# Kernel optimization log

Measured on AMD Instinct MI355X. Metric: run time of the kernel, lower is better.

## Reference

```python
import jax, jax.numpy as jnp
import numpy as np

N_NODES = 100000


def gcn_conv(x, src, dst, norm, W, b, n_nodes):
    # PyG GCNConv: h = x @ W; out[i] = sum_{j->i} norm_ij * h[j]; out += b
    h = x @ W  # [N, F_out]
    msg = h[src] * norm[:, None]  # [E+N, F_out] gather + scale
    out = jax.ops.segment_sum(msg, dst, num_segments=n_nodes)
    return out + b


def setup_inputs() -> dict:
    key = jax.random.key(0)
    ks = jax.random.split(key, 5)
    n, e = N_NODES, 1600000
    d_in, d_h, d_out = 512, 128, 40
    x = jax.random.normal(ks[0], (n, d_in), dtype=jnp.float32)
    edge_index = jax.random.randint(ks[1], (2, e), 0, n, dtype=jnp.int64)
    # Glorot-ish scaled weights
    W1 = jax.random.normal(ks[2], (d_in, d_h), dtype=jnp.float32) * (1.0 / np.sqrt(d_in))
    b1 = jnp.zeros((d_h,), dtype=jnp.float32)
    W2 = jax.random.normal(ks[3], (d_h, d_out), dtype=jnp.float32) * (1.0 / np.sqrt(d_h))
    b2 = jnp.zeros((d_out,), dtype=jnp.float32)
    return {"x": x, "edge_index": edge_index, "W1": W1, "b1": b1, "W2": W2, "b2": b2}


def reference(x, edge_index, W1, b1, W2, b2):
    n = x.shape[0]
    # add self-loops (PyG default add_self_loops=True)
    loop = jnp.arange(n, dtype=edge_index.dtype)
    src = jnp.concatenate([edge_index[0], loop])
    dst = jnp.concatenate([edge_index[1], loop])
    # symmetric normalization: deg^-1/2[src] * deg^-1/2[dst]
    deg = jax.ops.segment_sum(jnp.ones_like(dst, dtype=x.dtype), dst, num_segments=n)
    dinv = jnp.where(deg > 0, jax.lax.rsqrt(jnp.maximum(deg, 1.0)), 0.0)
    norm = dinv[src] * dinv[dst]
    h = gcn_conv(x, src, dst, norm, W1, b1, n)
    h = jax.nn.relu(h)
    h = gcn_conv(h, src, dst, norm, W2, b2, n)
    return jax.nn.log_softmax(h, axis=1)
```

## Files before the change

kernel.cpp:

```cpp
#include <hip/hip_runtime.h>
#include <math.h>

#define SCAN_B 512
#define NBSHIFT 8
#define CHUNK 8192

typedef __attribute__((ext_vector_type(8))) short short8;
typedef __attribute__((ext_vector_type(4))) float v4f;

__device__ __forceinline__ unsigned short f2bf(float f) {
    unsigned int u = __float_as_uint(f);
    u += 0x7FFFu + ((u >> 16) & 1u);
    return (unsigned short)(u >> 16);
}
__device__ __forceinline__ unsigned int packbf(float a, float b) {
    return (unsigned int)f2bf(a) | ((unsigned int)f2bf(b) << 16);
}
__device__ __forceinline__ void bf8_to_f32(uint4 v, float* f) {
    f[0] = __uint_as_float(v.x << 16); f[1] = __uint_as_float(v.x & 0xFFFF0000u);
    f[2] = __uint_as_float(v.y << 16); f[3] = __uint_as_float(v.y & 0xFFFF0000u);
    f[4] = __uint_as_float(v.z << 16); f[5] = __uint_as_float(v.z & 0xFFFF0000u);
    f[6] = __uint_as_float(v.w << 16); f[7] = __uint_as_float(v.w & 0xFFFF0000u);
}

__global__ void count_deg_kernel(const int* __restrict__ dst, int E, int* __restrict__ counts) {
    int e = blockIdx.x * blockDim.x + threadIdx.x;
    if (e < E) atomicAdd(&counts[dst[e]], 1);
}

__global__ void scan1_kernel(const int* __restrict__ counts, int N,
                             int* __restrict__ partial, int* __restrict__ blockSums) {
    __shared__ int sm[SCAN_B];
    int tid = threadIdx.x;
    int i = blockIdx.x * SCAN_B + tid;
    int v = (i < N) ? counts[i] : 0;
    sm[tid] = v;
    __syncthreads();
    for (int off = 1; off < SCAN_B; off <<= 1) {
        int t = (tid >= off) ? sm[tid - off] : 0;
        __syncthreads();
        sm[tid] += t;
        __syncthreads();
    }
    if (i < N) partial[i] = sm[tid] - v;
    if (tid == SCAN_B - 1) blockSums[blockIdx.x] = sm[tid];
}

__global__ void scan2_kernel(int* __restrict__ blockSums, int nb) {
    __shared__ int sm[256];
    int tid = threadIdx.x;
    int v = (tid < nb) ? blockSums[tid] : 0;
    sm[tid] = v;
    __syncthreads();
    for (int off = 1; off < 256; off <<= 1) {
        int t = (tid >= off) ? sm[tid - off] : 0;
        __syncthreads();
        sm[tid] += t;
        __syncthreads();
    }
    if (tid < nb) blockSums[tid] = sm[tid] - v;
}

__global__ void scan3_kernel(const int* __restrict__ counts, int* __restrict__ offsets,
                             const int* __restrict__ blockSums, int N, int E,
                             int* __restrict__ cursor, float* __restrict__ dinv) {
    int i = blockIdx.x * SCAN_B + threadIdx.x;
    if (i < N) {
        int off = offsets[i] + blockSums[blockIdx.x];
        offsets[i] = off;
        cursor[i] = off;
        dinv[i] = rsqrtf((float)(counts[i] + 1));
    }
    if (i == 0 && blockIdx.x == 0) offsets[N] = E;
}

__global__ void binbase_kernel(const int* __restrict__ offsets, int* __restrict__ bin_base,
                               int* __restrict__ bin_cursor, int nbins, int N) {
    int b = blockIdx.x * 256 + threadIdx.x;
    if (b <= nbins) {
        int node = b << NBSHIFT;
        if (node > N) node = N;
        bin_base[b] = offsets[node];
        if (b < nbins) bin_cursor[b] = offsets[node];
    }
}

__global__ __launch_bounds__(256) void binpass_kernel(const int* __restrict__ src,
                                                      const int* __restrict__ dst, int E,
                                                      int* __restrict__ bin_cursor,
                                                      unsigned int* __restrict__ bpairs, int nbins) {
    __shared__ unsigned int pk[CHUNK];
    __shared__ unsigned short binOf[CHUNK];
    __shared__ int hist[512];
    __shared__ int scanned[512];
    __shared__ int rank[512];
    __shared__ int gbase[512];
    int tid = threadIdx.x;
    int base = blockIdx.x * CHUNK;
    int cnt = E - base; if (cnt > CHUNK) cnt = CHUNK;

    for (int i = tid; i < 512; i += 256) { hist[i] = 0; rank[i] = 0; }
    __syncthreads();
    for (int i = tid; i < cnt; i += 256) {
        int d = dst[base + i];
        atomicAdd(&hist[d >> NBSHIFT], 1);
    }
    __syncthreads();
    scanned[tid] = hist[tid]; scanned[tid + 256] = hist[tid + 256];
    __syncthreads();
    for (int off = 1; off < 512; off <<= 1) {
        int i0 = tid, i1 = tid + 256;
        int v0 = (i0 >= off) ? scanned[i0 - off] : 0;
        int v1 = (i1 >= off) ? scanned[i1 - off] : 0;
        __syncthreads();
        scanned[i0] += v0; scanned[i1] += v1;
        __syncthreads();
    }
    for (int i = tid; i < cnt; i += 256) {
        int d = dst[base + i];
        int s = src[base + i];
        int b = d >> NBSHIFT;
        unsigned int p = (unsigned int)s | ((unsigned int)(d & 255) << 17);
        int r = atomicAdd(&rank[b], 1);
        int pos = scanned[b] - hist[b] + r;
        pk[pos] = p;
        binOf[pos] = (unsigned short)b;
    }
    __syncthreads();
    for (int b = tid; b < nbins; b += 256)
        if (hist[b] > 0) gbase[b] = atomicAdd(&bin_cursor[b], hist[b]);
    __syncthreads();
    for (int i = tid; i < cnt; i += 256) {
        int b = binOf[i];
        int local = i - (scanned[b] - hist[b]);
        bpairs[gbase[b] + local] = pk[i];
    }
}

__global__ __launch_bounds__(256) void binscatter_kernel(const unsigned int* __restrict__ bpairs,
                                                         const int* __restrict__ bin_base,
                                                         int* __restrict__ cursor,
                                                         int* __restrict__ ssrc) {
    int b = blockIdx.x;
    int start = bin_base[b], end = bin_base[b + 1];
    int dhigh = b << NBSHIFT;
    for (int i = start + threadIdx.x; i < end; i += 256) {
        unsigned int p = bpairs[i];
        int s = (int)(p & 0x1FFFFu);
        int d = dhigh | (int)(p >> 17);
        int pos = atomicAdd(&cursor[d], 1);
        ssrc[pos] = s;
    }
}

__global__ void w1cast_kernel(const float* __restrict__ W1, unsigned short* __restrict__ W1s) {
    int idx = blockIdx.x * 256 + threadIdx.x;
    int k = idx >> 7, n = idx & 127;
    int dstIdx = ((k >> 6) << 13) | (n << 6) | ((((k >> 3) & 7) ^ (n & 7)) << 3) | (k & 7);
    W1s[dstIdx] = f2bf(W1[idx]);
}

#define BM1 128
#define BK1 64

__global__ __launch_bounds__(256) void gemm1_mfma_kernel(const float* __restrict__ X,
                                                         const unsigned short* __restrict__ W1s,
                                                         unsigned short* __restrict__ H, int N) {
    __shared__ unsigned short SMEM[16384];
    unsigned short* As = SMEM;
    unsigned short* Bs = SMEM + 8192;
    int tid = threadIdx.x;
    int wave = tid >> 6, lane = tid & 63;
    int quad = lane >> 4, lr = lane & 15;
    int mBase = (wave & 1) * 64, nBase = (wave >> 1) * 64;
    int rowBase = blockIdx.x * BM1;

    v4f zero4 = {0.f, 0.f, 0.f, 0.f};
    v4f acc[4][4];
    #pragma unroll
    for (int i = 0; i < 4; i++)
        #pragma unroll
        for (int j = 0; j < 4; j++) acc[i][j] = zero4;

    float4 pfA0[4], pfA1[4];
    uint4  pfB[4];

    #define LOAD_A(K0)                                                                  \
        _Pragma("unroll")                                                               \
        for (int t = 0; t < 4; t++) {                                                   \
            int idx = tid + t * 256;                                                    \
            int r = idx >> 3, c = idx & 7;                                              \
            int gr = rowBase + r;                                                       \
            const float4* p = (const float4*)(X + (size_t)gr * 512 + (K0) + c * 8);     \
            bool ok = gr < N;                                                           \
            pfA0[t] = ok ? p[0] : make_float4(0.f, 0.f, 0.f, 0.f);                      \
            pfA1[t] = ok ? p[1] : make_float4(0.f, 0.f, 0.f, 0.f);                      \
        }
    #define LOAD_B(K0)                                                                  \
        _Pragma("unroll")                                                               \
        for (int t = 0; t < 4; t++)                                                     \
            pfB[t] = *(const uint4*)(W1s + (((K0) >> 6) << 13) + ((tid + t * 256) << 3));

    LOAD_A(0); LOAD_B(0);

    for (int k0 = 0; k0 < 512; k0 += BK1) {
        __syncthreads();
        #pragma unroll
        for (int t = 0; t < 4; t++) {
            int idx = tid + t * 256;
            int r = idx >> 3, c = idx & 7;
            uint4 v;
            v.x = packbf(pfA0[t].x, pfA0[t].y); v.y = packbf(pfA0[t].z, pfA0[t].w);
            v.z = packbf(pfA1[t].x, pfA1[t].y); v.w = packbf(pfA1[t].z, pfA1[t].w);
            *(uint4*)(&As[(r << 6) + ((c ^ (r & 7)) << 3)]) = v;
        }
        #pragma unroll
        for (int t = 0; t < 4; t++)
            *(uint4*)(&Bs[(tid + t * 256) << 3]) = pfB[t];
        __syncthreads();
        if (k0 + BK1 < 512) { LOAD_A(k0 + BK1); LOAD_B(k0 + BK1); }
        #pragma unroll
        for (int kc = 0; kc < BK1; kc += 32) {
            int cb = kc >> 3;
            short8 aF[4], bF[4];
            #pragma unroll
            for (int i = 0; i < 4; i++) {
                int m = mBase + i * 16 + lr;
                aF[i] = *(const short8*)(&As[m * 64 + (((cb + quad) ^ (m & 7)) << 3)]);
            }
            #pragma unroll
            for (int j = 0; j < 4; j++) {
                int n = nBase + j * 16 + lr;
                bF[j] = *(const short8*)(&Bs[n * 64 + (((cb + quad) ^ (n & 7)) << 3)]);
            }
            #pragma unroll
            for (int i = 0; i < 4; i++)
                #pragma unroll
                for (int j = 0; j < 4; j++)
                    acc[i][j] = __builtin_amdgcn_mfma_f32_16x16x32_bf16(aF[i], bF[j], acc[i][j], 0, 0, 0);
        }
    }
    __syncthreads();
    unsigned short* Cs = SMEM;
    #pragma unroll
    for (int i = 0; i < 4; i++) {
        #pragma unroll
        for (int r = 0; r < 4; r++) {
            int m = mBase + i * 16 + quad * 4 + r;
            #pragma unroll
            for (int j = 0; j < 4; j++)
                Cs[m * 128 + ((nBase + j * 16 + lr) ^ ((m & 7) << 4))] = f2bf(acc[i][j][r]);
        }
    }
    __syncthreads();
    #pragma unroll
    for (int t = 0; t < 8; t++) {
        int idx = tid + t * 256;
        int row = idx >> 4, c = idx & 15;
        int gr = rowBase + row;
        if (gr < N)
            *(uint4*)(H + (size_t)gr * 128 + c * 8) =
                *(const uint4*)(&Cs[row * 128 + ((c * 8) ^ ((row & 7) << 4))]);
    }
    #undef LOAD_A
    #undef LOAD_B
}

__global__ __launch_bounds__(256) void agg1_kernel(const unsigned short* __restrict__ h1,
                                                   const int* __restrict__ offsets,
                                                   const int* __restrict__ ssrc,
                                                   const float* __restrict__ dinv,
                                                   const float* __restrict__ bias,
                                                   unsigned short* __restrict__ a1, int N) {
    int lane = threadIdx.x & 15;
    int node = (blockIdx.x << 4) + (threadIdx.x >> 4);
    if (node >= N) return;
    const uint4* h = (const uint4*)h1;
    float di = dinv[node];
    float acc[8], t[8];
    bf8_to_f32(h[(size_t)node * 16 + lane], t);
    #pragma unroll
    for (int i = 0; i < 8; i++) acc[i] = di * t[i];
    int e = offsets[node], e1 = offsets[node + 1];
    for (; e + 3 < e1; e += 4) {
        int sA = ssrc[e], sB = ssrc[e + 1], sC = ssrc[e + 2], sD = ssrc[e + 3];
        float wA = dinv[sA], wB = dinv[sB], wC = dinv[sC], wD = dinv[sD];
        uint4 vA = h[(size_t)sA * 16 + lane];
        uint4 vB = h[(size_t)sB * 16 + lane];
        uint4 vC = h[(size_t)sC * 16 + lane];
        uint4 vD = h[(size_t)sD * 16 + lane];
        float fA[8], fB[8], fC[8], fD[8];
        bf8_to_f32(vA, fA); bf8_to_f32(vB, fB); bf8_to_f32(vC, fC); bf8_to_f32(vD, fD);
        #pragma unroll
        for (int i = 0; i < 8; i++) {
            acc[i] = fmaf(wA, fA[i], acc[i]);
            acc[i] = fmaf(wB, fB[i], acc[i]);
            acc[i] = fmaf(wC, fC[i], acc[i]);
            acc[i] = fmaf(wD, fD[i], acc[i]);
        }
    }
    for (; e < e1; e++) {
        int s = ssrc[e];
        float w = dinv[s];
        float fs[8];
        bf8_to_f32(h[(size_t)s * 16 + lane], fs);
        #pragma unroll
        for (int i = 0; i < 8; i++) acc[i] = fmaf(w, fs[i], acc[i]);
    }
    float4 b0 = ((const float4*)bias)[lane * 2];
    float4 b1v = ((const float4*)bias)[lane * 2 + 1];
    float bb[8] = {b0.x, b0.y, b0.z, b0.w, b1v.x, b1v.y, b1v.z, b1v.w};
    float o[8];
    #pragma unroll
    for (int i = 0; i < 8; i++) o[i] = fmaxf(fmaf(di, acc[i], bb[i]), 0.f);
    uint4 pv;
    pv.x = packbf(o[0], o[1]); pv.y = packbf(o[2], o[3]);
    pv.z = packbf(o[4], o[5]); pv.w = packbf(o[6], o[7]);
    ((uint4*)a1)[(size_t)node * 16 + lane] = pv;
}

__global__ __launch_bounds__(256) void gemm2_kernel(const unsigned short* __restrict__ A,
                                                    const float* __restrict__ W,
                                                    float* __restrict__ H, int N) {
    __shared__ float As2[128][64];
    __shared__ float Ws[128 * 40];
    int tid = threadIdx.x;
    int rowBase = blockIdx.x * 64;

    #pragma unroll
    for (int l = 0; l < 4; l++) {
        int e = tid + l * 256;
        int r = e >> 4;
        int kk = (e & 15) << 3;
        int grow = rowBase + r;
        float f[8] = {0.f, 0.f, 0.f, 0.f, 0.f, 0.f, 0.f, 0.f};
        if (grow < N) {
            uint4 v = *(const uint4*)(A + (size_t)grow * 128 + kk);
            bf8_to_f32(v, f);
        }
        #pragma unroll
        for (int q = 0; q < 8; q++) As2[kk + q][r] = f[q];
    }
    #pragma unroll
    for (int l = 0; l < 5; l++) {
        int e = tid + l * 256;
        *(float4*)&Ws[e << 2] = *(const float4*)&W[e << 2];
    }
    __syncthreads();

    int tx = tid & 7;
    int ty = tid >> 3;
    float acc[2][5];
    #pragma unroll
    for (int r = 0; r < 2; r++)
        #pragma unroll
        for (int c = 0; c < 5; c++) acc[r][c] = 0.f;

    #pragma unroll 8
    for (int k = 0; k < 128; k++) {
        float a0 = As2[k][ty * 2];
        float a1v = As2[k][ty * 2 + 1];
        #pragma unroll
        for (int c = 0; c < 5; c++) {
            float w = Ws[k * 40 + tx * 5 + c];
            acc[0][c] = fmaf(a0, w, acc[0][c]);
            acc[1][c] = fmaf(a1v, w, acc[1][c]);
        }
    }
    #pragma unroll
    for (int r = 0; r < 2; r++) {
        int grow = rowBase + ty * 2 + r;
        if (grow < N) {
            #pragma unroll
            for (int c = 0; c < 5; c++) H[grow * 40 + tx * 5 + c] = acc[r][c];
        }
    }
}

__global__ __launch_bounds__(256) void agg2_kernel(const float* __restrict__ h2,
                                                   const int* __restrict__ offsets,
                                                   const int* __restrict__ ssrc,
                                                   const float* __restrict__ dinv,
                                                   const float* __restrict__ bias,
                                                   float* __restrict__ out, int N) {
    int node = blockIdx.x * 4 + (threadIdx.x >> 6);
    int lane = threadIdx.x & 63;
    if (node >= N) return;
    float di = dinv[node];
    bool act = lane < 40;
    float acc = 0.f;
    if (act) acc = di * h2[(size_t)node * 40 + lane];
    int e = offsets[node], e1 = offsets[node + 1];
    for (; e + 3 < e1; e += 4) {
        int sa = ssrc[e], sb = ssrc[e + 1], sc = ssrc[e + 2], sd = ssrc[e + 3];
        float wa = dinv[sa], wb = dinv[sb], wc = dinv[sc], wd = dinv[sd];
        if (act) {
            float ha = h2[(size_t)sa * 40 + lane];
            float hb = h2[(size_t)sb * 40 + lane];
            float hc = h2[(size_t)sc * 40 + lane];
            float hd = h2[(size_t)sd * 40 + lane];
            acc = fmaf(wa, ha, acc); acc = fmaf(wb, hb, acc);
            acc = fmaf(wc, hc, acc); acc = fmaf(wd, hd, acc);
        }
    }
    for (; e < e1; e++) {
        int s = ssrc[e];
        float w = dinv[s];
        if (act) acc = fmaf(w, h2[(size_t)s * 40 + lane], acc);
    }
    float v = act ? fmaf(di, acc, bias[lane]) : -INFINITY;
    float m = v;
    #pragma unroll
    for (int off = 32; off; off >>= 1) m = fmaxf(m, __shfl_xor(m, off, 64));
    float ex = act ? expf(v - m) : 0.f;
    float s = ex;
    #pragma unroll
    for (int off = 32; off; off >>= 1) s += __shfl_xor(s, off, 64);
    if (act) out[(size_t)node * 40 + lane] = v - m - logf(s);
}

extern "C" void kernel_launch(void* const* d_in, const int* in_sizes, int n_in,
                              void* d_out, int out_size, void* d_ws, size_t ws_size,
                              hipStream_t stream) {
    const float* x  = (const float*)d_in[0];
    const int*   ei = (const int*)d_in[1];
    const float* W1 = (const float*)d_in[2];
    const float* b1 = (const float*)d_in[3];
    const float* W2 = (const float*)d_in[4];
    const float* b2 = (const float*)d_in[5];
    float* out = (float*)d_out;

    int N = in_sizes[0] / 512;
    int E = in_sizes[1] / 2;
    const int* src = ei;
    const int* dst = ei + E;
    int nbins = (N + 255) >> NBSHIFT;

    char* ws = (char*)d_ws;
    size_t off = 0;
    auto alloc = [&](size_t bytes) -> void* {
        void* p = ws + off;
        off += (bytes + 255) & ~(size_t)255;
        return p;
    };
    int*   counts    = (int*)alloc((size_t)N * 4);
    int*   offsets   = (int*)alloc((size_t)(N + 1) * 4);
    int*   cursor    = (int*)alloc((size_t)N * 4);
    float* dinv      = (float*)alloc((size_t)N * 4);
    int nb = (N + SCAN_B - 1) / SCAN_B;
    int*   blockSums = (int*)alloc((size_t)nb * 4);
    int*   bin_base  = (int*)alloc((size_t)(nbins + 1) * 4);
    int*   bin_cur   = (int*)alloc((size_t)nbins * 4);
    int*   ssrc      = (int*)alloc((size_t)E * 4);
    unsigned short* W1s = (unsigned short*)alloc((size_t)128 * 512 * 2);
    unsigned short* h1  = (unsigned short*)alloc((size_t)N * 128 * 2);
    unsigned short* a1  = (unsigned short*)alloc((size_t)N * 128 * 2);
    float* h2        = (float*)alloc((size_t)N * 40 * 4);
    unsigned int* bpairs = (unsigned int*)h1;
    (void)ws_size; (void)n_in; (void)out_size;

    hipMemsetAsync(counts, 0, (size_t)N * 4, stream);
    count_deg_kernel<<<(E + 255) / 256, 256, 0, stream>>>(dst, E, counts);
    scan1_kernel<<<nb, SCAN_B, 0, stream>>>(counts, N, offsets, blockSums);
    scan2_kernel<<<1, 256, 0, stream>>>(blockSums, nb);
    scan3_kernel<<<nb, SCAN_B, 0, stream>>>(counts, offsets, blockSums, N, E, cursor, dinv);
    binbase_kernel<<<(nbins + 256) / 256, 256, 0, stream>>>(offsets, bin_base, bin_cur, nbins, N);
    binpass_kernel<<<(E + CHUNK - 1) / CHUNK, 256, 0, stream>>>(src, dst, E, bin_cur, bpairs, nbins);
    binscatter_kernel<<<nbins, 256, 0, stream>>>(bpairs, bin_base, cursor, ssrc);
    w1cast_kernel<<<256, 256, 0, stream>>>(W1, W1s);
    gemm1_mfma_kernel<<<(N + BM1 - 1) / BM1, 256, 0, stream>>>(x, W1s, h1, N);
    agg1_kernel<<<(N + 15) / 16, 256, 0, stream>>>(h1, offsets, ssrc, dinv, b1, a1, N);
    gemm2_kernel<<<(N + 63) / 64, 256, 0, stream>>>(a1, W2, h2, N);
    agg2_kernel<<<(N + 3) / 4, 256, 0, stream>>>(h2, offsets, ssrc, dinv, b2, out, N);
}
```

Measured before the change: 646.8 us.

## Keep whole W1 resident in LDS with persistent 1024-thread GEMM1 blocks

Rewrites the first GEMM so each 1024-thread block loads all of W1 (bf16, 128 KiB, XOR-swizzled) into shared memory once. The blocks are persistent and loop over 256-row chunks, with each wave streaming its A rows straight from global memory into registers, converting them to bf16 and feeding MFMAs. This removes the per-tile B reloads, the A staging through LDS and most barriers. In exchange it uses 128 KiB of LDS, so only one block fits per CU, the grid is capped at 196, A loads go into registers without LDS reuse, and output stores become narrow 8-byte writes.

```diff
diff --git a/kernel.cpp b/kernel.cpp
--- a/kernel.cpp
+++ b/kernel.cpp
@@ -156,114 +156,81 @@
 __global__ void w1cast_kernel(const float* __restrict__ W1, unsigned short* __restrict__ W1s) {
     int idx = blockIdx.x * 256 + threadIdx.x;
     int k = idx >> 7, n = idx & 127;
-    int dstIdx = ((k >> 6) << 13) | (n << 6) | ((((k >> 3) & 7) ^ (n & 7)) << 3) | (k & 7);
-    W1s[dstIdx] = f2bf(W1[idx]);
-}
-
-#define BM1 128
-#define BK1 64
-
-__global__ __launch_bounds__(256) void gemm1_mfma_kernel(const float* __restrict__ X,
-                                                         const unsigned short* __restrict__ W1s,
-                                                         unsigned short* __restrict__ H, int N) {
-    __shared__ unsigned short SMEM[16384];
-    unsigned short* As = SMEM;
-    unsigned short* Bs = SMEM + 8192;
+    int us = (n * 512 + k) ^ ((n & 7) << 3);
+    W1s[us] = f2bf(W1[idx]);
+}
+
+__global__ __launch_bounds__(1024, 4) void gemm1_mfma_kernel(const float* __restrict__ X,
+                                                             const unsigned short* __restrict__ W1s,
+                                                             unsigned short* __restrict__ H,
+                                                             int N, int nChunks) {
+    extern __shared__ char smem[];
+    unsigned short* Bs = (unsigned short*)smem;
     int tid = threadIdx.x;
+    #pragma unroll
+    for (int i = 0; i < 8; i++)
+        ((uint4*)Bs)[tid + (i << 10)] = ((const uint4*)W1s)[tid + (i << 10)];
+    __syncthreads();
+
     int wave = tid >> 6, lane = tid & 63;
     int quad = lane >> 4, lr = lane & 15;
-    int mBase = (wave & 1) * 64, nBase = (wave >> 1) * 64;
-    int rowBase = blockIdx.x * BM1;
-
-    v4f zero4 = {0.f, 0.f, 0.f, 0.f};
-    v4f acc[4][4];
-    #pragma unroll
-    for (int i = 0; i < 4; i++)
-        #pragma unroll
-        for (int j = 0; j < 4; j++) acc[i][j] = zero4;
-
-    float4 pfA0[4], pfA1[4];
-    uint4  pfB[4];
-
-    #define LOAD_A(K0)                                                                  \
-        _Pragma("unroll")                                                               \
-        for (int t = 0; t < 4; t++) {                                                   \
-            int idx = tid + t * 256;                                                    \
-            int r = idx >> 3, c = idx & 7;                                              \
-            int gr = rowBase + r;                                                       \
-            const float4* p = (const float4*)(X + (size_t)gr * 512 + (K0) + c * 8);     \
-            bool ok = gr < N;                                                           \
-            pfA0[t] = ok ? p[0] : make_float4(0.f, 0.f, 0.f, 0.f);                      \
-            pfA1[t] = ok ? p[1] : make_float4(0.f, 0.f, 0.f, 0.f);                      \
-        }
-    #define LOAD_B(K0)                                                                  \
-        _Pragma("unroll")                                                               \
-        for (int t = 0; t < 4; t++)                                                     \
-            pfB[t] = *(const uint4*)(W1s + (((K0) >> 6) << 13) + ((tid + t * 256) << 3));
-
-    LOAD_A(0); LOAD_B(0);
-
-    for (int k0 = 0; k0 < 512; k0 += BK1) {
-        __syncthreads();
-        #pragma unroll
-        for (int t = 0; t < 4; t++) {
-            int idx = tid + t * 256;
-            int r = idx >> 3, c = idx & 7;
-            uint4 v;
-            v.x = packbf(pfA0[t].x, pfA0[t].y); v.y = packbf(pfA0[t].z, pfA0[t].w);
-            v.z = packbf(pfA1[t].x, pfA1[t].y); v.w = packbf(pfA1[t].z, pfA1[t].w);
-            *(uint4*)(&As[(r << 6) + ((c ^ (r & 7)) << 3)]) = v;
-        }
-        #pragma unroll
-        for (int t = 0; t < 4; t++)
-            *(uint4*)(&Bs[(tid + t * 256) << 3]) = pfB[t];
-        __syncthreads();
-        if (k0 + BK1 < 512) { LOAD_A(k0 + BK1); LOAD_B(k0 + BK1); }
-        #pragma unroll
-        for (int kc = 0; kc < BK1; kc += 32) {
-            int cb = kc >> 3;
-            short8 aF[4], bF[4];
-            #pragma unroll
-            for (int i = 0; i < 4; i++) {
-                int m = mBase + i * 16 + lr;
-                aF[i] = *(const short8*)(&As[m * 64 + (((cb + quad) ^ (m & 7)) << 3)]);
+    const char* spRow = smem + lr * 1024;
+    const char* sp0 = spRow + ((quad * 16) ^ ((lr & 7) << 4));
+    const char* sp1 = spRow + ((quad * 16 + 64) ^ ((lr & 7) << 4));
+
+    for (int c = 0;; c++) {
+        int chunk = blockIdx.x + c * gridDim.x;
+        if (chunk >= nChunks) break;
+        int row = (chunk << 8) + (wave << 4) + lr;
+        int rowc = row < N ? row : N - 1;
+        const float* pA = X + (size_t)rowc * 512 + quad * 8;
+        float4 pf0 = *(const float4*)(pA);
+        float4 pf1 = *(const float4*)(pA + 4);
+        float4 pf2 = *(const float4*)(pA + 32);
+        float4 pf3 = *(const float4*)(pA + 36);
+        v4f acc[8];
+        #pragma unroll
+        for (int j = 0; j < 8; j++) acc[j] = (v4f){0.f, 0.f, 0.f, 0.f};
+
+        #pragma unroll
+        for (int ks = 0; ks < 8; ks++) {
+            uint4 ua, ub;
+            ua.x = packbf(pf0.x, pf0.y); ua.y = packbf(pf0.z, pf0.w);
+            ua.z = packbf(pf1.x, pf1.y); ua.w = packbf(pf1.z, pf1.w);
+            ub.x = packbf(pf2.x, pf2.y); ub.y = packbf(pf2.z, pf2.w);
+            ub.z = packbf(pf3.x, pf3.y); ub.w = packbf(pf3.z, pf3.w);
+            short8 aF0, aF1;
+            *(uint4*)&aF0 = ua;
+            *(uint4*)&aF1 = ub;
+            if (ks < 7) {
+                int k0 = ks * 64;
+                pf0 = *(const float4*)(pA + k0 + 64);
+                pf1 = *(const float4*)(pA + k0 + 68);
+                pf2 = *(const float4*)(pA + k0 + 96);
+                pf3 = *(const float4*)(pA + k0 + 100);
             }
             #pragma unroll
-            for (int j = 0; j < 4; j++) {
-                int n = nBase + j * 16 + lr;
-                bF[j] = *(const short8*)(&Bs[n * 64 + (((cb + quad) ^ (n & 7)) << 3)]);
+            for (int j = 0; j < 8; j++) {
+                short8 bF = *(const short8*)(sp0 + j * 16384 + ks * 128);
+                acc[j] = __builtin_amdgcn_mfma_f32_16x16x32_bf16(bF, aF0, acc[j], 0, 0, 0);
             }
             #pragma unroll
-            for (int i = 0; i < 4; i++)
-                #pragma unroll
-                for (int j = 0; j < 4; j++)
-                    acc[i][j] = __builtin_amdgcn_mfma_f32_16x16x32_bf16(aF[i], bF[j], acc[i][j], 0, 0, 0);
-        }
-    }
-    __syncthreads();
-    unsigned short* Cs = SMEM;
-    #pragma unroll
-    for (int i = 0; i < 4; i++) {
-        #pragma unroll
-        for (int r = 0; r < 4; r++) {
-            int m = mBase + i * 16 + quad * 4 + r;
+            for (int j = 0; j < 8; j++) {
+                short8 bF = *(const short8*)(sp1 + j * 16384 + ks * 128);
+                acc[j] = __builtin_amdgcn_mfma_f32_16x16x32_bf16(bF, aF1, acc[j], 0, 0, 0);
+            }
+        }
+        if (row < N) {
+            unsigned short* pH = H + (size_t)row * 128 + quad * 4;
             #pragma unroll
-            for (int j = 0; j < 4; j++)
-                Cs[m * 128 + ((nBase + j * 16 + lr) ^ ((m & 7) << 4))] = f2bf(acc[i][j][r]);
-        }
-    }
-    __syncthreads();
-    #pragma unroll
-    for (int t = 0; t < 8; t++) {
-        int idx = tid + t * 256;
-        int row = idx >> 4, c = idx & 15;
-        int gr = rowBase + row;
-        if (gr < N)
-            *(uint4*)(H + (size_t)gr * 128 + c * 8) =
-                *(const uint4*)(&Cs[row * 128 + ((c * 8) ^ ((row & 7) << 4))]);
-    }
-    #undef LOAD_A
-    #undef LOAD_B
+            for (int j = 0; j < 8; j++) {
+                ushort4 o;
+                o.x = f2bf(acc[j][0]); o.y = f2bf(acc[j][1]);
+                o.z = f2bf(acc[j][2]); o.w = f2bf(acc[j][3]);
+                *(ushort4*)(pH + j * 16) = o;
+            }
+        }
+    }
 }
 
 __global__ __launch_bounds__(256) void agg1_kernel(const unsigned short* __restrict__ h1,
@@ -468,7 +435,9 @@
     binpass_kernel<<<(E + CHUNK - 1) / CHUNK, 256, 0, stream>>>(src, dst, E, bin_cur, bpairs, nbins);
     binscatter_kernel<<<nbins, 256, 0, stream>>>(bpairs, bin_base, cursor, ssrc);
     w1cast_kernel<<<256, 256, 0, stream>>>(W1, W1s);
-    gemm1_mfma_kernel<<<(N + BM1 - 1) / BM1, 256, 0, stream>>>(x, W1s, h1, N);
+    int nChunks = (N + 255) >> 8;
+    int g1grid = nChunks < 196 ? nChunks : 196;
+    gemm1_mfma_kernel<<<g1grid, 1024, 131072, stream>>>(x, W1s, h1, N, nChunks);
     agg1_kernel<<<(N + 15) / 16, 256, 0, stream>>>(h1, offsets, ssrc, dinv, b1, a1, N);
     gemm2_kernel<<<(N + 63) / 64, 256, 0, stream>>>(a1, W2, h2, N);
     agg2_kernel<<<(N + 3) / 4, 256, 0, stream>>>(h2, offsets, ssrc, dinv, b2, out, N);
```

Result: slower. 896.5 us (+38.6%).
